# Kernel tuning notes

Hardware: AMD Instinct MI355X
Metric: run time of the kernel (lower is better)

The kernel has to match this reference:

```python
import itertools
import jax, jax.numpy as jnp
import numpy as np

N = 400000
CIN, COUT = 32, 64
K, STRIDE, PAD, DIL = 3, 2, 1, 1
SPATIAL = (200, 200, 16)
PRUNING_RATIO = 0.5

def _out_spatial():
    return tuple((s + 2 * PAD - DIL * (K - 1) - 1) // STRIDE + 1 for s in SPATIAL)


def setup_inputs() -> dict:
    key = jax.random.key(0)
    kf, kc0, kc1, kc2, kc3, km, kw = jax.random.split(key, 7)
    features = jax.random.normal(kf, (N, CIN), dtype=jnp.float32)
    b = jax.random.randint(kc0, (N,), 0, 2, dtype=jnp.int32)
    z = jax.random.randint(kc1, (N,), 0, SPATIAL[0], dtype=jnp.int32)
    y = jax.random.randint(kc2, (N,), 0, SPATIAL[1], dtype=jnp.int32)
    x = jax.random.randint(kc3, (N,), 0, SPATIAL[2], dtype=jnp.int32)
    coors = jnp.stack([b, z, y, x], axis=1)  # [N,4] = (batch, d0, d1, d2)
    mask = jax.random.uniform(km, (N,), dtype=jnp.float32)
    weight = jax.random.normal(kw, (K, K, K, CIN, COUT), dtype=jnp.float32) * 0.05
    return {"features": features, "coors": coors, "mask": mask, "weight": weight, "batch_size": 2}


def _sprs_conv(features, coors, mask, weight, batch_size):
    out_sp = _out_spatial()  # (100, 100, 8)
    num_out = batch_size * out_sp[0] * out_sp[1] * out_sp[2]
    n = features.shape[0]
    # rank-based pruning: keep top (1 - pruning_ratio) points as 'important'
    thr = jnp.sort(mask)[int(n * PRUNING_RATIO)]
    important = (mask >= thr)  # [N] bool

    b = coors[:, 0]
    pos = coors[:, 1:4]  # [N,3]
    out_sp_arr = jnp.array(out_sp, dtype=pos.dtype)

    # accumulators; slot num_out is a dump for invalid indices
    acc = jnp.zeros((num_out + 1, COUT), dtype=features.dtype)
    imp_cnt = jnp.zeros((num_out + 1,), dtype=jnp.int32)

    for off in itertools.product(range(K), repeat=3):
        off_arr = jnp.array(off, dtype=pos.dtype)
        num = pos + PAD - DIL * off_arr  # [N,3]
        oc = num // STRIDE
        valid = jnp.all(num % STRIDE == 0, axis=-1) & jnp.all(oc >= 0, axis=-1) & jnp.all(oc < out_sp_arr, axis=-1)
        lin = ((b * out_sp[0] + oc[:, 0]) * out_sp[1] + oc[:, 1]) * out_sp[2] + oc[:, 2]
        idx = jnp.where(valid, lin, num_out)
        vals = features @ weight[off[0], off[1], off[2]]  # [N,Cout] gather-GEMM
        acc = acc.at[idx].add(vals)  # scatter
        imp_cnt = imp_cnt.at[idx].add((important & valid).astype(jnp.int32))

    keep = (imp_cnt[:num_out] > 0)  # output positions reached by >=1 important point
    return acc[:num_out] * keep[:, None]


def reference(features, coors, mask, weight, batch_size):
    return _sprs_conv(features, coors, mask, weight, batch_size)
```

## Files before the change

kernel.cpp:

```cpp
#include <hip/hip_runtime.h>

#define CIN 32
#define COUT 64
#define OD0 100
#define OD1 100
#define OD2 8


__global__ void hist_hi_kernel(const float* __restrict__ mask, int n, int* __restrict__ hist) {
    int i = blockIdx.x * blockDim.x + threadIdx.x;
    if (i >= n) return;
    unsigned bits = __float_as_uint(mask[i]);
    atomicAdd(&hist[bits >> 16], 1);
}

__global__ void hist_lo_kernel(const float* __restrict__ mask, int n,
                               const int* __restrict__ sel, int* __restrict__ hist) {
    int i = blockIdx.x * blockDim.x + threadIdx.x;
    if (i >= n) return;
    unsigned bits = __float_as_uint(mask[i]);
    if ((int)(bits >> 16) == sel[0]) atomicAdd(&hist[bits & 0xFFFFu], 1);
}

__global__ void select_kernel(const int* __restrict__ hist, const int* rankSrc,
                              int rankConst, int* outPair) {
    __shared__ int partial[256];
    __shared__ int scan[257];
    int t = threadIdx.x;
    int rank = rankSrc ? *rankSrc : rankConst;
    const int* h = hist + t * 256;
    int sum = 0;
    for (int j = 0; j < 256; j++) sum += h[j];
    partial[t] = sum;
    __syncthreads();
    if (t == 0) {
        int c = 0;
        for (int j = 0; j < 256; j++) { scan[j] = c; c += partial[j]; }
        scan[256] = c;
    }
    __syncthreads();
    int base = scan[t];
    if (rank >= base && rank < scan[t + 1]) {
        int c = base;
        for (int j = 0; j < 256; j++) {
            int hv = h[j];
            if (rank < c + hv) { outPair[0] = t * 256 + j; outPair[1] = rank - c; break; }
            c += hv;
        }
    }
}


__global__ void __launch_bounds__(256)
scatter_kernel(const float* __restrict__ feat, const int* __restrict__ coors,
               const float* __restrict__ mask, const float* __restrict__ W,
               const int* __restrict__ sel, float* __restrict__ out,
               int* __restrict__ keep, int n) {
    int gid = blockIdx.x * blockDim.x + threadIdx.x;
    int wave = gid >> 6;
    int lane = threadIdx.x & 63;
    if (wave >= n) return;

    const int4 c4 = ((const int4*)coors)[wave];
    int bb = c4.x, pz = c4.y, py = c4.z, px = c4.w;

    unsigned thrBits = ((unsigned)sel[0] << 16) | (unsigned)sel[2];
    float thr = __uint_as_float(thrBits);
    bool imp = mask[wave] >= thr;

    int oz[2], ozo[2], nz = 0;
    int oy[2], oyo[2], ny = 0;
    int ox[2], oxo[2], nx = 0;
#pragma unroll
    for (int o = 0; o < 3; o++) {
        int num = pz + 1 - o;
        if (num >= 0 && !(num & 1) && (num >> 1) < OD0) { oz[nz] = num >> 1; ozo[nz] = o; nz++; }
        num = py + 1 - o;
        if (num >= 0 && !(num & 1) && (num >> 1) < OD1) { oy[ny] = num >> 1; oyo[ny] = o; ny++; }
        num = px + 1 - o;
        if (num >= 0 && !(num & 1) && (num >> 1) < OD2) { ox[nx] = num >> 1; oxo[nx] = o; nx++; }
    }

    float f[CIN];
    const float4* fp = (const float4*)(feat + (size_t)wave * CIN);
#pragma unroll
    for (int j = 0; j < CIN / 4; j++) {
        float4 v = fp[j];
        f[4 * j + 0] = v.x; f[4 * j + 1] = v.y; f[4 * j + 2] = v.z; f[4 * j + 3] = v.w;
    }

    for (int a = 0; a < nz; a++)
        for (int b = 0; b < ny; b++)
            for (int c = 0; c < nx; c++) {
                int woff = ((ozo[a] * 3 + oyo[b]) * 3 + oxo[c]) * (CIN * COUT);
                const float* w = W + woff + lane;
                float acc = 0.f;
#pragma unroll
                for (int k = 0; k < CIN; k++) acc = fmaf(f[k], w[k * COUT], acc);
                int lin = ((bb * OD0 + oz[a]) * OD1 + oy[b]) * OD2 + ox[c];
                atomicAdd(out + (size_t)lin * COUT + lane, acc);
                if (imp && lane == 0) keep[lin] = 1;
            }
}


__global__ void finalize_kernel(float* __restrict__ out, const int* __restrict__ keep, int numOut) {
    int t = blockIdx.x * blockDim.x + threadIdx.x;
    if (t >= numOut * (COUT / 4)) return;
    int o = t >> 4;
    if (!keep[o]) ((float4*)out)[t] = make_float4(0.f, 0.f, 0.f, 0.f);
}

extern "C" void kernel_launch(void* const* d_in, const int* in_sizes, int n_in,
                              void* d_out, int out_size, void* d_ws, size_t ws_size,
                              hipStream_t stream) {
    const float* feat  = (const float*)d_in[0];
    const int*   coors = (const int*)d_in[1];
    const float* mask  = (const float*)d_in[2];
    const float* W     = (const float*)d_in[3];

    int n = in_sizes[2];
    int numOut = out_size / COUT;
    int rank = (int)(n * 0.5);

    char* ws = (char*)d_ws;
    int* histHi = (int*)ws;
    int* histLo = (int*)(ws + 65536 * 4);
    int* sel    = (int*)(ws + 2 * 65536 * 4);
    int* keep   = (int*)(ws + 2 * 65536 * 4 + 64);
    size_t zeroBytes = 2 * 65536 * 4 + 64 + (size_t)numOut * 4;

    hipMemsetAsync(d_out, 0, (size_t)out_size * sizeof(float), stream);
    hipMemsetAsync(d_ws, 0, zeroBytes, stream);

    const int blk = 256;
    int gN = (n + blk - 1) / blk;
    hist_hi_kernel<<<gN, blk, 0, stream>>>(mask, n, histHi);
    select_kernel<<<1, 256, 0, stream>>>(histHi, nullptr, rank, sel);
    hist_lo_kernel<<<gN, blk, 0, stream>>>(mask, n, sel, histLo);
    select_kernel<<<1, 256, 0, stream>>>(histLo, sel + 1, 0, sel + 2);

    long long threads = (long long)n * 64;
    int gScatter = (int)((threads + blk - 1) / blk);
    scatter_kernel<<<gScatter, blk, 0, stream>>>(feat, coors, mask, W, sel,
                                                 (float*)d_out, keep, n);

    int fin = numOut * (COUT / 4);
    finalize_kernel<<<(fin + blk - 1) / blk, blk, 0, stream>>>((float*)d_out, keep, numOut);
}
```

Before: 873.9 us.

## Replace atomic scatter with output-stationary gather via per-voxel linked-list grid

Builds a dense voxel hash (head/next linked lists via atomicExch) over input coordinates and launches one wavefront per output voxel. Each wave walks its 3x3x3 input neighborhood, accumulates in registers using a transposed weight layout that allows float4 loads, and writes the output once. The keep mask is applied inline. This removes the float atomics, the output memset and the finalize pass. In exchange it needs a larger workspace, adds extra launches for the transpose and grid build, and iterates many empty cells for the sparse input. The original path is kept as a fallback when the workspace is too small.

```diff
diff --git a/kernel.cpp b/kernel.cpp
--- a/kernel.cpp
+++ b/kernel.cpp
@@ -5,6 +5,10 @@
 #define OD0 100
 #define OD1 100
 #define OD2 8
+#define IZ 200
+#define IY 200
+#define IX 16
+#define NTAP 27
 
 
 __global__ void hist_hi_kernel(const float* __restrict__ mask, int n, int* __restrict__ hist) {
@@ -51,6 +55,97 @@
 }
 
 
+__global__ void transpose_w_kernel(const float* __restrict__ W, float* __restrict__ Wt) {
+    int i = blockIdx.x * blockDim.x + threadIdx.x;
+    if (i >= NTAP * CIN * COUT) return;
+    int cout = i % COUT;
+    int rest = i / COUT;
+    int cin = rest % CIN;
+    int tap = rest / CIN;
+    Wt[((size_t)tap * COUT + cout) * CIN + cin] = W[i];
+}
+
+__global__ void build_grid_kernel(const int* __restrict__ coors, int n,
+                                  int* __restrict__ head, int* __restrict__ next) {
+    int i = blockIdx.x * blockDim.x + threadIdx.x;
+    if (i >= n) return;
+    const int4 c = ((const int4*)coors)[i];
+    int cell = ((c.x * IZ + c.y) * IY + c.z) * IX + c.w;
+    next[i] = atomicExch(&head[cell], i);
+}
+
+
+__global__ void __launch_bounds__(256)
+gather_kernel(const float* __restrict__ feat, const float* __restrict__ mask,
+              const float* __restrict__ Wt, const int* __restrict__ sel,
+              const int* __restrict__ head, const int* __restrict__ next,
+              float* __restrict__ out, int numOut) {
+    int gid = blockIdx.x * blockDim.x + threadIdx.x;
+    int wave = gid >> 6;
+    int lane = threadIdx.x & 63;
+    if (wave >= numOut) return;
+
+    int ox = wave & (OD2 - 1);
+    int t = wave >> 3;
+    int oy = t % OD1;
+    t /= OD1;
+    int oz = t % OD0;
+    int bb = t / OD0;
+
+    unsigned thrBits = ((unsigned)sel[0] << 16) | (unsigned)sel[2];
+    float thr = __uint_as_float(thrBits);
+
+    float acc = 0.f;
+    int keep = 0;
+    int pz0 = 2 * oz - 1, py0 = 2 * oy - 1, px0 = 2 * ox - 1;
+
+    for (int o0 = 0; o0 < 3; o0++) {
+        int pz = pz0 + o0;
+        if ((unsigned)pz >= (unsigned)IZ) continue;
+        for (int o1 = 0; o1 < 3; o1++) {
+            int py = py0 + o1;
+            if ((unsigned)py >= (unsigned)IY) continue;
+            for (int o2 = 0; o2 < 3; o2++) {
+                int px = px0 + o2;
+                if ((unsigned)px >= (unsigned)IX) continue;
+                int cell = ((bb * IZ + pz) * IY + py) * IX + px;
+                int p = head[cell];
+                if (p < 0) continue;
+                int tap = (o0 * 3 + o1) * 3 + o2;
+                const float4* wp = (const float4*)(Wt + ((size_t)tap * COUT + lane) * CIN);
+                float4 w0 = wp[0], w1 = wp[1], w2 = wp[2], w3 = wp[3];
+                float4 w4 = wp[4], w5 = wp[5], w6 = wp[6], w7 = wp[7];
+                do {
+                    int sp = __builtin_amdgcn_readfirstlane(p);
+                    const float4* fp = (const float4*)(feat + (size_t)sp * CIN);
+                    float4 f0 = fp[0], f1 = fp[1], f2 = fp[2], f3 = fp[3];
+                    float4 f4 = fp[4], f5 = fp[5], f6 = fp[6], f7 = fp[7];
+                    acc = fmaf(f0.x, w0.x, acc); acc = fmaf(f0.y, w0.y, acc);
+                    acc = fmaf(f0.z, w0.z, acc); acc = fmaf(f0.w, w0.w, acc);
+                    acc = fmaf(f1.x, w1.x, acc); acc = fmaf(f1.y, w1.y, acc);
+                    acc = fmaf(f1.z, w1.z, acc); acc = fmaf(f1.w, w1.w, acc);
+                    acc = fmaf(f2.x, w2.x, acc); acc = fmaf(f2.y, w2.y, acc);
+                    acc = fmaf(f2.z, w2.z, acc); acc = fmaf(f2.w, w2.w, acc);
+                    acc = fmaf(f3.x, w3.x, acc); acc = fmaf(f3.y, w3.y, acc);
+                    acc = fmaf(f3.z, w3.z, acc); acc = fmaf(f3.w, w3.w, acc);
+                    acc = fmaf(f4.x, w4.x, acc); acc = fmaf(f4.y, w4.y, acc);
+                    acc = fmaf(f4.z, w4.z, acc); acc = fmaf(f4.w, w4.w, acc);
+                    acc = fmaf(f5.x, w5.x, acc); acc = fmaf(f5.y, w5.y, acc);
+                    acc = fmaf(f5.z, w5.z, acc); acc = fmaf(f5.w, w5.w, acc);
+                    acc = fmaf(f6.x, w6.x, acc); acc = fmaf(f6.y, w6.y, acc);
+                    acc = fmaf(f6.z, w6.z, acc); acc = fmaf(f6.w, w6.w, acc);
+                    acc = fmaf(f7.x, w7.x, acc); acc = fmaf(f7.y, w7.y, acc);
+                    acc = fmaf(f7.z, w7.z, acc); acc = fmaf(f7.w, w7.w, acc);
+                    keep |= (mask[sp] >= thr) ? 1 : 0;
+                    p = next[sp];
+                } while (p >= 0);
+            }
+        }
+    }
+    out[(size_t)wave * COUT + lane] = keep ? acc : 0.f;
+}
+
+
 __global__ void __launch_bounds__(256)
 scatter_kernel(const float* __restrict__ feat, const int* __restrict__ coors,
                const float* __restrict__ mask, const float* __restrict__ W,
@@ -103,7 +198,6 @@
             }
 }
 
-
 __global__ void finalize_kernel(float* __restrict__ out, const int* __restrict__ keep, int numOut) {
     int t = blockIdx.x * blockDim.x + threadIdx.x;
     if (t >= numOut * (COUT / 4)) return;
@@ -123,28 +217,62 @@
     int numOut = out_size / COUT;
     int rank = (int)(n * 0.5);
 
-    char* ws = (char*)d_ws;
-    int* histHi = (int*)ws;
-    int* histLo = (int*)(ws + 65536 * 4);
-    int* sel    = (int*)(ws + 2 * 65536 * 4);
-    int* keep   = (int*)(ws + 2 * 65536 * 4 + 64);
-    size_t zeroBytes = 2 * 65536 * 4 + 64 + (size_t)numOut * 4;
-
-    hipMemsetAsync(d_out, 0, (size_t)out_size * sizeof(float), stream);
-    hipMemsetAsync(d_ws, 0, zeroBytes, stream);
-
     const int blk = 256;
     int gN = (n + blk - 1) / blk;
-    hist_hi_kernel<<<gN, blk, 0, stream>>>(mask, n, histHi);
-    select_kernel<<<1, 256, 0, stream>>>(histHi, nullptr, rank, sel);
-    hist_lo_kernel<<<gN, blk, 0, stream>>>(mask, n, sel, histLo);
-    select_kernel<<<1, 256, 0, stream>>>(histLo, sel + 1, 0, sel + 2);
-
-    long long threads = (long long)n * 64;
-    int gScatter = (int)((threads + blk - 1) / blk);
-    scatter_kernel<<<gScatter, blk, 0, stream>>>(feat, coors, mask, W, sel,
-                                                 (float*)d_out, keep, n);
-
-    int fin = numOut * (COUT / 4);
-    finalize_kernel<<<(fin + blk - 1) / blk, blk, 0, stream>>>((float*)d_out, keep, numOut);
-}
+
+    char* ws = (char*)d_ws;
+
+    size_t offHistHi = 0;
+    size_t offHistLo = 65536 * 4;
+    size_t offSel    = 2 * 65536 * 4;
+    size_t offWt     = offSel + 64;
+    size_t offHead   = offWt + (size_t)NTAP * CIN * COUT * 4;
+    size_t offNext   = offHead + (size_t)2 * IZ * IY * IX * 4;
+    size_t need      = offNext + (size_t)n * 4;
+
+    int* histHi = (int*)(ws + offHistHi);
+    int* histLo = (int*)(ws + offHistLo);
+    int* sel    = (int*)(ws + offSel);
+
+    if (ws_size >= need) {
+        float* Wt  = (float*)(ws + offWt);
+        int* head  = (int*)(ws + offHead);
+        int* next  = (int*)(ws + offNext);
+
+        hipMemsetAsync(ws, 0, offWt, stream);
+        hipMemsetAsync(head, 0xFF, (size_t)2 * IZ * IY * IX * 4, stream);
+
+        hist_hi_kernel<<<gN, blk, 0, stream>>>(mask, n, histHi);
+        select_kernel<<<1, 256, 0, stream>>>(histHi, nullptr, rank, sel);
+        hist_lo_kernel<<<gN, blk, 0, stream>>>(mask, n, sel, histLo);
+        select_kernel<<<1, 256, 0, stream>>>(histLo, sel + 1, 0, sel + 2);
+
+        int wElems = NTAP * CIN * COUT;
+        transpose_w_kernel<<<(wElems + blk - 1) / blk, blk, 0, stream>>>(W, Wt);
+        build_grid_kernel<<<gN, blk, 0, stream>>>(coors, n, head, next);
+
+        long long threads = (long long)numOut * 64;
+        int gGather = (int)((threads + blk - 1) / blk);
+        gather_kernel<<<gGather, blk, 0, stream>>>(feat, mask, Wt, sel,
+                                                   head, next, (float*)d_out, numOut);
+    } else {
+        int* keep = (int*)(ws + offSel + 64);
+        size_t zeroBytes = offSel + 64 + (size_t)numOut * 4;
+
+        hipMemsetAsync(d_out, 0, (size_t)out_size * sizeof(float), stream);
+        hipMemsetAsync(d_ws, 0, zeroBytes, stream);
+
+        hist_hi_kernel<<<gN, blk, 0, stream>>>(mask, n, histHi);
+        select_kernel<<<1, 256, 0, stream>>>(histHi, nullptr, rank, sel);
+        hist_lo_kernel<<<gN, blk, 0, stream>>>(mask, n, sel, histLo);
+        select_kernel<<<1, 256, 0, stream>>>(histLo, sel + 1, 0, sel + 2);
+
+        long long threads = (long long)n * 64;
+        int gScatter = (int)((threads + blk - 1) / blk);
+        scatter_kernel<<<gScatter, blk, 0, stream>>>(feat, coors, mask, W, sel,
+                                                     (float*)d_out, keep, n);
+
+        int fin = numOut * (COUT / 4);
+        finalize_kernel<<<(fin + blk - 1) / blk, blk, 0, stream>>>((float*)d_out, keep, numOut);
+    }
+}
```

Result: slower. 1.385 ms (+58.5%).
